# Kernel optimization log

Measured on AMD Instinct MI355X. Metric: run time of the kernel, lower is better.

## Reference

```python
import jax, jax.numpy as jnp
import numpy as np

N = 16384      # total nodes in batched graph
B = 64         # number of graphs (dgl.batch)
DEG = 8        # random in-degree (self-loops added on top)
C = 128        # feature width
H = 2          # heads in middle blocks
EH = 8         # E: heads of attn_seq / codebook entries
DEPTH = 2
IN = 8         # max_node_color (one-hot input width)
NE = N * DEG + N  # edges incl. self-loops


def layernorm(x, g, b, eps=1e-5):
    mu = jnp.mean(x, axis=-1, keepdims=True)
    var = jnp.mean(jnp.square(x - mu), axis=-1, keepdims=True)
    return (x - mu) * jax.lax.rsqrt(var + eps) * g + b


def gatv2(x, src, dst, Ws, bs, Wd, bd, attn):
    # DGL GATv2Conv (eval mode, attn_drop inactive, share_weights=False)
    h, c = attn.shape
    n = x.shape[0]
    el = (x @ Ws + bs).reshape(n, h, c)   # fc_src
    er = (x @ Wd + bd).reshape(n, h, c)   # fc_dst
    e = jax.nn.leaky_relu(el[src] + er[dst], negative_slope=0.2)  # [E,h,c]
    logits = jnp.einsum('ehc,hc->eh', e, attn)                    # [E,h]
    # edge softmax over incoming edges of each dst node
    m = jax.ops.segment_max(logits, dst, num_segments=n)
    a = jnp.exp(logits - m[dst])
    z = jax.ops.segment_sum(a, dst, num_segments=n)
    a = a / z[dst]
    return jax.ops.segment_sum(el[src] * a[..., None], dst, num_segments=n)  # [n,h,c]


def setup_inputs() -> dict:
    key = jax.random.key(0)
    ks = iter(jax.random.split(key, 64))
    nrm = lambda *s: jax.random.normal(next(ks), s, jnp.float32) * 0.05
    colors = jax.random.randint(next(ks), (N,), 0, IN)
    feats = jax.nn.one_hot(colors, IN, dtype=jnp.float32)
    loops = jnp.arange(N)
    src = jnp.concatenate([jax.random.randint(next(ks), (N * DEG,), 0, N), loops])
    dst = jnp.concatenate([jax.random.randint(next(ks), (N * DEG,), 0, N), loops])
    graph_ids = jnp.arange(N) // (N // B)
    inp = dict(feats=feats, src=src, dst=dst, graph_ids=graph_ids)
    # attn_up: GATv2Conv(IN -> C, 1 head)
    inp.update(up_Ws=nrm(IN, C), up_bs=nrm(C), up_Wd=nrm(IN, C), up_bd=nrm(C), up_attn=nrm(1, C))
    # depth blocks: GATv2Conv(C -> C, H heads) + ff
    inp.update(L_Ws=nrm(DEPTH, C, H * C), L_bs=nrm(DEPTH, H * C),
               L_Wd=nrm(DEPTH, C, H * C), L_bd=nrm(DEPTH, H * C),
               L_attn=nrm(DEPTH, H, C),
               ff_ln_g=jnp.ones((DEPTH, C), jnp.float32), ff_ln_b=jnp.zeros((DEPTH, C), jnp.float32),
               ff_W1=nrm(DEPTH, C, 2 * C), ff_b1=nrm(DEPTH, 2 * C),
               ff_W2=nrm(DEPTH, 2 * C, C), ff_b2=nrm(DEPTH, C),
               ff_W3=nrm(DEPTH, H * C, C), ff_b3=nrm(DEPTH, C))
    # attn_seq: GATv2Conv(C -> C, EH heads) + ff_seq
    inp.update(seq_Ws=nrm(C, EH * C), seq_bs=nrm(EH * C),
               seq_Wd=nrm(C, EH * C), seq_bd=nrm(EH * C),
               seq_attn=nrm(EH, C),
               fs_ln_g=jnp.ones((C,), jnp.float32), fs_ln_b=jnp.zeros((C,), jnp.float32),
               fs_W1=nrm(C, 2 * C), fs_b1=nrm(2 * C),
               fs_W2=nrm(2 * C, C), fs_b2=nrm(C),
               gate_W=nrm(EH * C, 1), gate_b=nrm(1))
    return inp


def reference(feats, src, dst, graph_ids,
              up_Ws, up_bs, up_Wd, up_bd, up_attn,
              L_Ws, L_bs, L_Wd, L_bd, L_attn,
              ff_ln_g, ff_ln_b, ff_W1, ff_b1, ff_W2, ff_b2, ff_W3, ff_b3,
              seq_Ws, seq_bs, seq_Wd, seq_bd, seq_attn,
              fs_ln_g, fs_ln_b, fs_W1, fs_b1, fs_W2, fs_b2,
              gate_W, gate_b):
    # attn_up (1 head) -> flatten to [N, C]
    x = gatv2(feats, src, dst, up_Ws, up_bs, up_Wd, up_bd, up_attn).reshape(N, C)
    for l in range(DEPTH):
        h = gatv2(x, src, dst, L_Ws[l], L_bs[l], L_Wd[l], L_bd[l], L_attn[l])  # [N,H,C]
        h = layernorm(h, ff_ln_g[l], ff_ln_b[l])
        h = jax.nn.gelu(h @ ff_W1[l] + ff_b1[l], approximate=False)
        h = h @ ff_W2[l] + ff_b2[l]                              # [N,H,C]
        x = h.reshape(N, H * C) @ ff_W3[l] + ff_b3[l]            # [N,C]
    y = gatv2(x, src, dst, seq_Ws, seq_bs, seq_Wd, seq_bd, seq_attn)  # [N,EH,C]
    y = layernorm(y, fs_ln_g, fs_ln_b)
    y = jax.nn.gelu(y @ fs_W1 + fs_b1, approximate=False) @ fs_W2 + fs_b2
    y = y.reshape(N, EH * C)
    # GlobalAttentionPooling: softmax(gate) over nodes within each graph
    gate = y @ gate_W + gate_b                                   # [N,1]
    gm = jax.ops.segment_max(gate, graph_ids, num_segments=B)
    ga = jnp.exp(gate - gm[graph_ids])
    gz = jax.ops.segment_sum(ga, graph_ids, num_segments=B)
    ga = ga / gz[graph_ids]
    pooled = jax.ops.segment_sum(ga * y, graph_ids, num_segments=B)  # [B, EH*C]
    return jnp.tanh(pooled.reshape(B, EH, C))
```

## Files before the change

kernel.cpp:

```cpp
#include <hip/hip_runtime.h>
#include <hip/hip_bf16.h>

typedef __hip_bfloat16 bf16;
typedef __attribute__((ext_vector_type(8))) short short8;
typedef __attribute__((ext_vector_type(4))) float f32x4;

#define NN 16384
#define NB 64
#define NE_TOT (NN*8 + NN)
#define CW 128

__device__ __forceinline__ float b2f(bf16 x){ return __bfloat162float(x); }
__device__ __forceinline__ bf16  f2b(float x){ return __float2bfloat16(x); }
__device__ __forceinline__ float lrelu(float x){ return fmaxf(x, 0.2f*x); }
__device__ __forceinline__ float gelu_f(float x){ return 0.5f*x*(1.f + erff(x*0.70710678118654752f)); }
__device__ __forceinline__ float us2f(unsigned int u){ return __uint_as_float(u << 16); }
__device__ __forceinline__ unsigned short f2us(float x){ return __builtin_bit_cast(unsigned short, f2b(x)); }

__device__ __forceinline__ void async16(const void* g, void* l){
  __builtin_amdgcn_global_load_lds((const __attribute__((address_space(1))) void*)g,
                                   (__attribute__((address_space(3))) void*)l, 16, 0, 0);
}

__global__ void k_detect(const unsigned short* __restrict__ f, int* __restrict__ flag){
  __shared__ int cnt;
  if(threadIdx.x == 0) cnt = 0;
  __syncthreads();
  int c = 0;
  for(int i = threadIdx.x; i < 2048; i += 256)
    if(f[2*i] == 0x3F80) c++;
  atomicAdd(&cnt, c);
  __syncthreads();
  if(threadIdx.x == 0) *flag = (cnt > 0) ? 0 : 1;
}

struct ConvArgs { const void* in[32]; bf16* out[32]; int n[32]; int tk[32]; int tj[32]; int ls[32]; };
__global__ __launch_bounds__(256) void k_conv_all(ConvArgs a, const int* __restrict__ flag){
  int which = blockIdx.y;
  int t = blockIdx.x*256 + threadIdx.x;
  int n = a.n[which];
  if(t >= n) return;
  float v = (*flag) ? ((const float*)a.in[which])[t] : b2f(((const bf16*)a.in[which])[t]);
  int tj = a.tj[which];
  if(tj == 0){ a.out[which][t] = f2b(v); return; }
  int tk = a.tk[which], kj = tk*tj;
  int l = t / kj, r = t - l*kj;
  int k = r / tj, j = r - k*tj;
  a.out[which][l*a.ls[which] + j*tk + k] = f2b(v);
}

__global__ void k_zero3(int* __restrict__ a, int* __restrict__ b, float* __restrict__ g, int n){
  int i = blockIdx.x*blockDim.x + threadIdx.x;
  if(i < n){ a[i] = 0; b[i] = 0; g[i] = 0.f; }
}
__global__ void k_hist(const int* __restrict__ dst, int* __restrict__ deg, int ne){
  int e = blockIdx.x*blockDim.x + threadIdx.x;
  if(e < ne) atomicAdd(&deg[dst[e]], 1);
}
__global__ void k_scan(const int* __restrict__ deg, int* __restrict__ off){
  __shared__ int s[256];
  int t = threadIdx.x;
  const int chunk = NN/256;
  int base = t*chunk;
  int sum = 0;
  for(int i=0;i<chunk;i++) sum += deg[base+i];
  s[t] = sum; __syncthreads();
  for(int o=1;o<256;o<<=1){
    int v = (t >= o) ? s[t-o] : 0;
    __syncthreads();
    s[t] += v;
    __syncthreads();
  }
  int run = (t == 0) ? 0 : s[t-1];
  for(int i=0;i<chunk;i++){ off[base+i] = run; run += deg[base+i]; }
  if(t == 255) off[NN] = run;
}
__global__ void k_scatter(const int* __restrict__ src, const int* __restrict__ dst,
                          const int* __restrict__ off, int* __restrict__ cursor,
                          int* __restrict__ csr_src, int ne){
  int e = blockIdx.x*blockDim.x + threadIdx.x;
  if(e < ne){
    int d = dst[e];
    int p = off[d] + atomicAdd(&cursor[d], 1);
    csr_src[p] = src[e];
  }
}

__global__ __launch_bounds__(128) void k_up(const bf16* __restrict__ feats,
    const bf16* __restrict__ Ws, const bf16* __restrict__ bs,
    const bf16* __restrict__ Wd, const bf16* __restrict__ bd,
    bf16* __restrict__ eler){
  int n = blockIdx.x, c = threadIdx.x;
  __shared__ float f[8];
  if(c < 8) f[c] = b2f(feats[n*8 + c]);
  __syncthreads();
  float a = b2f(bs[c]), b = b2f(bd[c]);
  #pragma unroll
  for(int k=0;k<8;k++){
    float fv = f[k];
    a += fv*b2f(Ws[k*CW + c]);
    b += fv*b2f(Wd[k*CW + c]);
  }
  eler[(size_t)n*256 + c]       = f2b(a);
  eler[(size_t)n*256 + 128 + c] = f2b(b);
}

template<int ACT>
__global__ __launch_bounds__(256) void k_mm(
    const bf16* __restrict__ A, int gshA, int gstrA,
    const bf16* __restrict__ WT, const bf16* __restrict__ bias,
    bf16* __restrict__ C, int gshC, int gstrC,
    int K, int J){
  __shared__ char smem[32768];
  short* As = (short*)smem;
  short* Bs = (short*)(smem + 16384);
  int tid = threadIdx.x, w = tid >> 6, lane = tid & 63;
  int l15 = lane & 15, q = lane >> 4;
  int wm = w >> 1, wn = w & 1;
  int bm = blockIdx.y*128, bn = blockIdx.x*128;

  f32x4 acc[4][4];
  #pragma unroll
  for(int i=0;i<4;i++)
    #pragma unroll
    for(int j=0;j<4;j++) acc[i][j] = (f32x4)0.f;

  int srow = w*32 + (lane >> 2);
  int scol = (lane & 3)*8;
  const bf16* gA[2]; const bf16* gB[2];
  short* lA[2]; short* lB[2];
  int mskA = (1 << gshA) - 1;
  #pragma unroll
  for(int a=0;a<2;a++){
    int rowA = bm + srow + a*16;
    gA[a] = A  + (size_t)(rowA >> gshA)*(size_t)gstrA + (size_t)(rowA & mskA)*K + scol;
    gB[a] = WT + (size_t)(bn + srow + a*16)*K + scol;
    lA[a] = As + (w*32 + a*16)*32;
    lB[a] = Bs + (w*32 + a*16)*32;
  }

  for(int kt=0; kt<K; kt+=64){
    #pragma unroll
    for(int a=0;a<2;a++)
      #pragma unroll
      for(int kh=0;kh<2;kh++){
        async16(gA[a] + kt + kh*32, lA[a] + kh*4096);
        async16(gB[a] + kt + kh*32, lB[a] + kh*4096);
      }
    __syncthreads();
    #pragma unroll
    for(int kh=0;kh<2;kh++){
      short8 af[4], bfr[4];
      #pragma unroll
      for(int i=0;i<4;i++) af[i]  = *(short8*)&As[kh*4096 + (wm*64 + i*16 + l15)*32 + q*8];
      #pragma unroll
      for(int j=0;j<4;j++) bfr[j] = *(short8*)&Bs[kh*4096 + (wn*64 + j*16 + l15)*32 + q*8];
      #pragma unroll
      for(int i=0;i<4;i++)
        #pragma unroll
        for(int j=0;j<4;j++)
          acc[i][j] = __builtin_amdgcn_mfma_f32_16x16x32_bf16(af[i], bfr[j], acc[i][j], 0, 0, 0);
    }
    __syncthreads();
  }

  float* ep = (float*)(smem + w*4352);
  int rr = lane >> 2;
  int cc = (lane & 3)*16;
  int mskC = (1 << gshC) - 1;
  #pragma unroll
  for(int i=0;i<4;i++){
    #pragma unroll
    for(int j=0;j<4;j++){
      float bv = b2f(bias[bn + wn*64 + j*16 + l15]);
      #pragma unroll
      for(int r=0;r<4;r++){
        float v = acc[i][j][r] + bv;
        if(ACT == 1) v = gelu_f(v);
        ep[(q*4+r)*68 + j*16 + l15] = v;
      }
    }
    float4 v0 = *(float4*)&ep[rr*68 + cc];
    float4 v1 = *(float4*)&ep[rr*68 + cc + 4];
    float4 v2 = *(float4*)&ep[rr*68 + cc + 8];
    float4 v3 = *(float4*)&ep[rr*68 + cc + 12];
    float vv[16] = {v0.x,v0.y,v0.z,v0.w, v1.x,v1.y,v1.z,v1.w,
                    v2.x,v2.y,v2.z,v2.w, v3.x,v3.y,v3.z,v3.w};
    unsigned int u[8];
    #pragma unroll
    for(int k=0;k<8;k++)
      u[k] = (unsigned int)f2us(vv[2*k]) | ((unsigned int)f2us(vv[2*k+1]) << 16);
    int row = bm + wm*64 + i*16 + rr;
    bf16* cp = C + (size_t)(row >> gshC)*(size_t)gstrC + (size_t)(row & mskC)*J + bn + wn*64 + cc;
    *(uint4*)cp       = make_uint4(u[0],u[1],u[2],u[3]);
    *(uint4*)(cp + 8) = make_uint4(u[4],u[5],u[6],u[7]);
  }
}

template<int E>
__device__ __forceinline__ void load_row(const bf16* p, float* f){
  if constexpr (E == 2){
    unsigned int v = *(const unsigned int*)p;
    f[0] = us2f(v & 0xffffu); f[1] = __uint_as_float(v & 0xffff0000u);
  } else if constexpr (E == 4){
    uint2 v = *(const uint2*)p;
    f[0] = us2f(v.x & 0xffffu); f[1] = __uint_as_float(v.x & 0xffff0000u);
    f[2] = us2f(v.y & 0xffffu); f[3] = __uint_as_float(v.y & 0xffff0000u);
  } else if constexpr (E == 8){
    uint4 a = *(const uint4*)p;
    unsigned int vs[4] = {a.x,a.y,a.z,a.w};
    #pragma unroll
    for(int i=0;i<4;i++){
      f[2*i]   = us2f(vs[i] & 0xffffu);
      f[2*i+1] = __uint_as_float(vs[i] & 0xffff0000u);
    }
  } else {
    uint4 a = *(const uint4*)p;
    uint4 b = *(const uint4*)(p + 8);
    unsigned int vs[8] = {a.x,a.y,a.z,a.w,b.x,b.y,b.z,b.w};
    #pragma unroll
    for(int i=0;i<8;i++){
      f[2*i]   = us2f(vs[i] & 0xffffu);
      f[2*i+1] = __uint_as_float(vs[i] & 0xffff0000u);
    }
  }
}
template<int E>
__device__ __forceinline__ void store_row(bf16* p, const float* f){
  unsigned int vs[E/2];
  #pragma unroll
  for(int i=0;i<E/2;i++)
    vs[i] = (unsigned int)f2us(f[2*i]) | ((unsigned int)f2us(f[2*i+1]) << 16);
  if constexpr (E == 2){ *(unsigned int*)p = vs[0]; }
  else if constexpr (E == 4){ *(uint2*)p = make_uint2(vs[0], vs[1]); }
  else if constexpr (E == 8){ *(uint4*)p = make_uint4(vs[0], vs[1], vs[2], vs[3]); }
  else {
    *(uint4*)p       = make_uint4(vs[0], vs[1], vs[2], vs[3]);
    *(uint4*)(p + 8) = make_uint4(vs[4], vs[5], vs[6], vs[7]);
  }
}

template<int GATE>
__global__ __launch_bounds__(256) void k_ff(
    const bf16* __restrict__ A, int gshA, int gstrA,
    const bf16* __restrict__ W1T, const bf16* __restrict__ b1,
    const bf16* __restrict__ W2T, const bf16* __restrict__ b2,
    bf16* __restrict__ C, int gshC, int gstrC,
    const bf16* __restrict__ gW, float* __restrict__ gate){
  __shared__ short Wb[8704];
  __shared__ short Hs[16896];
  int tid = threadIdx.x, w = tid >> 6, lane = tid & 63;
  int l15 = lane & 15, q = lane >> 4;
  int bm = blockIdx.x*64;
  int mskA = (1 << gshA) - 1, mskC = (1 << gshC) - 1;

  int rowA = bm + w*16 + l15;
  const bf16* ap = A + (size_t)(rowA >> gshA)*(size_t)gstrA + (size_t)(rowA & mskA)*128;
  short8 af[4];
  #pragma unroll
  for(int ki=0;ki<4;ki++) af[ki] = *(const short8*)&ap[ki*32 + q*8];

  for(int jt=0; jt<4; jt++){
    #pragma unroll
    for(int it=0;it<4;it++){
      int slot = tid + it*256;
      int r = slot >> 4, c8 = slot & 15;
      *(int4*)&Wb[r*132 + c8*8] = *(const int4*)&W1T[(size_t)(jt*64 + r)*128 + c8*8];
    }
    __syncthreads();
    f32x4 acc1[4] = {(f32x4)0.f, (f32x4)0.f, (f32x4)0.f, (f32x4)0.f};
    #pragma unroll
    for(int ki=0;ki<4;ki++){
      #pragma unroll
      for(int t=0;t<4;t++){
        short8 bfr = *(short8*)&Wb[(t*16 + l15)*132 + ki*32 + q*8];
        acc1[t] = __builtin_amdgcn_mfma_f32_16x16x32_bf16(af[ki], bfr, acc1[t], 0, 0, 0);
      }
    }
    #pragma unroll
    for(int t=0;t<4;t++){
      int jcol = jt*64 + t*16 + l15;
      float bv = b2f(b1[jcol]);
      #pragma unroll
      for(int r=0;r<4;r++){
        float v = gelu_f(acc1[t][r] + bv);
        Hs[(w*16 + q*4 + r)*260 + jcol] = (short)f2us(v);
      }
    }
    __syncthreads();
  }

  f32x4 acc2[8];
  #pragma unroll
  for(int t=0;t<8;t++) acc2[t] = (f32x4)0.f;
  for(int kc=0; kc<4; kc++){
    #pragma unroll
    for(int it=0;it<4;it++){
      int slot = tid + it*256;
      int r = slot >> 3, c8 = slot & 7;
      *(int4*)&Wb[r*68 + c8*8] = *(const int4*)&W2T[(size_t)r*256 + kc*64 + c8*8];
    }
    __syncthreads();
    #pragma unroll
    for(int ki=0;ki<2;ki++){
      short8 haf = *(short8*)&Hs[(w*16 + l15)*260 + kc*64 + ki*32 + q*8];
      #pragma unroll
      for(int t=0;t<8;t++){
        short8 bfr = *(short8*)&Wb[(t*16 + l15)*68 + ki*32 + q*8];
        acc2[t] = __builtin_amdgcn_mfma_f32_16x16x32_bf16(haf, bfr, acc2[t], 0, 0, 0);
      }
    }
    __syncthreads();
  }

  float* epf = (float*)Hs;
  #pragma unroll
  for(int t=0;t<8;t++){
    int jcol = t*16 + l15;
    float bv = b2f(b2[jcol]);
    #pragma unroll
    for(int r=0;r<4;r++)
      epf[(w*16 + q*4 + r)*132 + jcol] = acc2[t][r] + bv;
  }
  __syncthreads();
  int row = tid >> 2, cseg = (tid & 3)*32;
  float vv[32];
  #pragma unroll
  for(int k8=0;k8<8;k8++){
    float4 v = *(float4*)&epf[row*132 + cseg + k8*4];
    vv[k8*4+0] = v.x; vv[k8*4+1] = v.y; vv[k8*4+2] = v.z; vv[k8*4+3] = v.w;
  }
  unsigned int u[16];
  #pragma unroll
  for(int k=0;k<16;k++)
    u[k] = (unsigned int)f2us(vv[2*k]) | ((unsigned int)f2us(vv[2*k+1]) << 16);
  int rowC = bm + row;
  bf16* cpb = C + (size_t)(rowC >> gshC)*(size_t)gstrC + (size_t)(rowC & mskC)*128 + cseg;
  *(uint4*)cpb        = make_uint4(u[0], u[1], u[2], u[3]);
  *(uint4*)(cpb + 8)  = make_uint4(u[4], u[5], u[6], u[7]);
  *(uint4*)(cpb + 16) = make_uint4(u[8], u[9], u[10],u[11]);
  *(uint4*)(cpb + 24) = make_uint4(u[12],u[13],u[14],u[15]);

  if constexpr (GATE){
    float gwf[32];
    load_row<16>(gW + (rowC & 7)*128 + cseg,      gwf);
    load_row<16>(gW + (rowC & 7)*128 + cseg + 16, gwf + 16);
    float p = 0.f;
    #pragma unroll
    for(int k=0;k<32;k++) p += vv[k]*gwf[k];
    p += __shfl_xor(p, 1, 64);
    p += __shfl_xor(p, 2, 64);
    if((tid & 3) == 0) atomicAdd(&gate[rowC >> 3], p);
  }
}

__global__ __launch_bounds__(256) void k_ffw3(
    const bf16* __restrict__ A,
    const bf16* __restrict__ W1T, const bf16* __restrict__ b1,
    const bf16* __restrict__ W2T, const bf16* __restrict__ b2,
    const bf16* __restrict__ W3T, const bf16* __restrict__ b3,
    bf16* __restrict__ X){
  __shared__ short Wb[8704];
  __shared__ short Hs[16896];
  int tid = threadIdx.x, w = tid >> 6, lane = tid & 63;
  int l15 = lane & 15, q = lane >> 4;
  int bm = blockIdx.x*64;

  int rowA = bm + w*16 + l15;
  const bf16* ap = A + (size_t)rowA*128;
  short8 af[4];
  #pragma unroll
  for(int ki=0;ki<4;ki++) af[ki] = *(const short8*)&ap[ki*32 + q*8];

  for(int jt=0; jt<4; jt++){
    #pragma unroll
    for(int it=0;it<4;it++){
      int slot = tid + it*256;
      int r = slot >> 4, c8 = slot & 15;
      *(int4*)&Wb[r*132 + c8*8] = *(const int4*)&W1T[(size_t)(jt*64 + r)*128 + c8*8];
    }
    __syncthreads();
    f32x4 acc1[4] = {(f32x4)0.f, (f32x4)0.f, (f32x4)0.f, (f32x4)0.f};
    #pragma unroll
    for(int ki=0;ki<4;ki++){
      #pragma unroll
      for(int t=0;t<4;t++){
        short8 bfr = *(short8*)&Wb[(t*16 + l15)*132 + ki*32 + q*8];
        acc1[t] = __builtin_amdgcn_mfma_f32_16x16x32_bf16(af[ki], bfr, acc1[t], 0, 0, 0);
      }
    }
    #pragma unroll
    for(int t=0;t<4;t++){
      int jcol = jt*64 + t*16 + l15;
      float bv = b2f(b1[jcol]);
      #pragma unroll
      for(int r=0;r<4;r++){
        float v = gelu_f(acc1[t][r] + bv);
        Hs[(w*16 + q*4 + r)*260 + jcol] = (short)f2us(v);
      }
    }
    __syncthreads();
  }

  f32x4 acc2[8];
  #pragma unroll
  for(int t=0;t<8;t++) acc2[t] = (f32x4)0.f;
  for(int kc=0; kc<4; kc++){
    #pragma unroll
    for(int it=0;it<4;it++){
      int slot = tid + it*256;
      int r = slot >> 3, c8 = slot & 7;
      *(int4*)&Wb[r*68 + c8*8] = *(const int4*)&W2T[(size_t)r*256 + kc*64 + c8*8];
    }
    __syncthreads();
    #pragma unroll
    for(int ki=0;ki<2;ki++){
      short8 haf = *(short8*)&Hs[(w*16 + l15)*260 + kc*64 + ki*32 + q*8];
      #pragma unroll
      for(int t=0;t<8;t++){
        short8 bfr = *(short8*)&Wb[(t*16 + l15)*68 + ki*32 + q*8];
        acc2[t] = __builtin_amdgcn_mfma_f32_16x16x32_bf16(haf, bfr, acc2[t], 0, 0, 0);
      }
    }
    __syncthreads();
  }
  #pragma unroll
  for(int t=0;t<8;t++){
    int jcol = t*16 + l15;
    float bv = b2f(b2[jcol]);
    #pragma unroll
    for(int r=0;r<4;r++)
      Wb[(w*16 + q*4 + r)*128 + jcol] = (short)f2us(acc2[t][r] + bv);
  }
  __syncthreads();

  int mt = w >> 1, jh = w & 1;
  short8 a3[8];
  #pragma unroll
  for(int c=0;c<8;c++) a3[c] = *(short8*)&Wb[(mt*16 + l15)*256 + c*32 + q*8];
  __syncthreads();

  f32x4 acc3[4] = {(f32x4)0.f, (f32x4)0.f, (f32x4)0.f, (f32x4)0.f};
  for(int kc=0; kc<4; kc++){
    #pragma unroll
    for(int it=0;it<4;it++){
      int slot = tid + it*256;
      int r = slot >> 3, c8 = slot & 7;
      *(int4*)&Wb[r*68 + c8*8] = *(const int4*)&W3T[(size_t)r*256 + kc*64 + c8*8];
    }
    __syncthreads();
    #pragma unroll
    for(int ki=0;ki<2;ki++){
      short8 haf = a3[kc*2 + ki];
      #pragma unroll
      for(int t=0;t<4;t++){
        short8 bfr = *(short8*)&Wb[(jh*64 + t*16 + l15)*68 + ki*32 + q*8];
        acc3[t] = __builtin_amdgcn_mfma_f32_16x16x32_bf16(haf, bfr, acc3[t], 0, 0, 0);
      }
    }
    __syncthreads();
  }

  float* epf = (float*)Hs;
  #pragma unroll
  for(int t=0;t<4;t++){
    int jcol = jh*64 + t*16 + l15;
    float bv = b2f(b3[jcol]);
    #pragma unroll
    for(int r=0;r<4;r++)
      epf[(mt*16 + q*4 + r)*132 + jcol] = acc3[t][r] + bv;
  }
  __syncthreads();
  int row = tid >> 3, cseg = (tid & 7)*16;
  float4 v0 = *(float4*)&epf[row*132 + cseg];
  float4 v1 = *(float4*)&epf[row*132 + cseg + 4];
  float4 v2 = *(float4*)&epf[row*132 + cseg + 8];
  float4 v3 = *(float4*)&epf[row*132 + cseg + 12];
  float vv[16] = {v0.x,v0.y,v0.z,v0.w, v1.x,v1.y,v1.z,v1.w,
                  v2.x,v2.y,v2.z,v2.w, v3.x,v3.y,v3.z,v3.w};
  unsigned int u[8];
  #pragma unroll
  for(int k=0;k<8;k++)
    u[k] = (unsigned int)f2us(vv[2*k]) | ((unsigned int)f2us(vv[2*k+1]) << 16);
  bf16* xp = X + (size_t)(bm/2 + row)*128 + cseg;
  *(uint4*)xp       = make_uint4(u[0],u[1],u[2],u[3]);
  *(uint4*)(xp + 8) = make_uint4(u[4],u[5],u[6],u[7]);
}

template<int H, bool LNF>
__global__ __launch_bounds__(256) void k_gat(const int* __restrict__ off, const int* __restrict__ csr_src,
    const bf16* __restrict__ el, const bf16* __restrict__ er, const bf16* __restrict__ attn,
    const bf16* __restrict__ lng, const bf16* __restrict__ lnb, bf16* __restrict__ out,
    int rs_in, int rs_out){
  constexpr int EPL = 2*H;
  constexpr int G   = 64/H;
  int w = threadIdx.x >> 6, lane = threadIdx.x & 63;
  int n = blockIdx.x*4 + w;

  float ef[EPL], af[EPL];
  load_row<EPL>(er   + (size_t)n*rs_in + lane*EPL, ef);
  load_row<EPL>(attn + lane*EPL, af);

  int p0 = off[n], p1 = off[n+1];
  int deg = p1 - p0;
  int sidx = csr_src[p0 + (lane < deg ? lane : deg-1)];

  float z = 0.f;
  float acc[EPL];
  #pragma unroll
  for(int e=0;e<EPL;e++) acc[e] = 0.f;

  float xa[EPL], xb[EPL];
  {
    int s0 = __shfl(sidx, 0, 64);
    load_row<EPL>(el + (size_t)s0*rs_in + lane*EPL, xa);
  }
  if(deg > 1){
    int s1 = __shfl(sidx, 1, 64);
    load_row<EPL>(el + (size_t)s1*rs_in + lane*EPL, xb);
  }

  for(int p = 0; p < deg; p += 2){
    float na[EPL], nb[EPL];
    int i2 = p + 2, i3 = p + 3;
    int s2b = __shfl(sidx, i2 & 63, 64);
    int s3b = __shfl(sidx, i3 & 63, 64);
    if(i2 < deg){
      int sc = (i2 < 64) ? s2b : csr_src[p0 + i2];
      load_row<EPL>(el + (size_t)sc*rs_in + lane*EPL, na);
    }
    if(i3 < deg){
      int sd = (i3 < 64) ? s3b : csr_src[p0 + i3];
      load_row<EPL>(el + (size_t)sd*rs_in + lane*EPL, nb);
    }
    {
      float part = 0.f;
      #pragma unroll
      for(int e=0;e<EPL;e++) part += af[e]*lrelu(xa[e] + ef[e]);
      #pragma unroll
      for(int o=G/2; o; o>>=1) part += __shfl_xor(part, o, 64);
      float c = __expf(part);
      z += c;
      #pragma unroll
      for(int e=0;e<EPL;e++) acc[e] += c*xa[e];
    }
    if(p + 1 < deg){
      float part = 0.f;
      #pragma unroll
      for(int e=0;e<EPL;e++) part += af[e]*lrelu(xb[e] + ef[e]);
      #pragma unroll
      for(int o=G/2; o; o>>=1) part += __shfl_xor(part, o, 64);
      float c = __expf(part);
      z += c;
      #pragma unroll
      for(int e=0;e<EPL;e++) acc[e] += c*xb[e];
    }
    #pragma unroll
    for(int e=0;e<EPL;e++){ xa[e] = na[e]; xb[e] = nb[e]; }
  }
  float rz = 1.f/z;
  #pragma unroll
  for(int e=0;e<EPL;e++) acc[e] *= rz;

  if constexpr (LNF){
    float sl = 0.f;
    #pragma unroll
    for(int e=0;e<EPL;e++) sl += acc[e];
    #pragma unroll
    for(int o=G/2; o; o>>=1) sl += __shfl_xor(sl, o, 64);
    float mu = sl*(1.f/128.f);
    float qs = 0.f;
    #pragma unroll
    for(int e=0;e<EPL;e++){ float d = acc[e] - mu; qs += d*d; }
    #pragma unroll
    for(int o=G/2; o; o>>=1) qs += __shfl_xor(qs, o, 64);
    float r = rsqrtf(qs*(1.f/128.f) + 1e-5f);
    int cbase = (lane & (G-1))*EPL;
    #pragma unroll
    for(int e=0;e<EPL;e++)
      acc[e] = (acc[e] - mu)*r*b2f(lng[cbase + e]) + b2f(lnb[cbase + e]);
  }
  store_row<EPL>(out + (size_t)n*rs_out + lane*EPL, acc);
}

__global__ __launch_bounds__(64) void k_pool1(const float* __restrict__ gate,
                                              float* __restrict__ gm, float* __restrict__ gz){
  int g = blockIdx.x, lane = threadIdx.x;
  float v0 = gate[g*256 + lane], v1 = gate[g*256 + 64 + lane];
  float v2 = gate[g*256 + 128 + lane], v3 = gate[g*256 + 192 + lane];
  float m = fmaxf(fmaxf(v0,v1), fmaxf(v2,v3));
  #pragma unroll
  for(int o=32;o;o>>=1) m = fmaxf(m, __shfl_xor(m, o, 64));
  float z = __expf(v0-m) + __expf(v1-m) + __expf(v2-m) + __expf(v3-m);
  #pragma unroll
  for(int o=32;o;o>>=1) z += __shfl_xor(z, o, 64);
  if(lane == 0){ gm[g] = m; gz[g] = z; }
}

__global__ __launch_bounds__(256) void k_pool2(const float* __restrict__ gate,
    const float* __restrict__ gm, const float* __restrict__ gz,
    const bf16* __restrict__ y2, void* __restrict__ outv, const int* __restrict__ flag){
  int g = blockIdx.x >> 2, cb = blockIdx.x & 3, t = threadIdx.x;
  __shared__ float aL[256];
  aL[t] = __expf(gate[g*256 + t] - gm[g]) / gz[g];
  __syncthreads();
  int ch = cb*256 + t;
  float acc = 0.f;
  const bf16* base = y2 + (size_t)g*256*2048 + ch;
  for(int i=0;i<256;i++) acc += aL[i]*b2f(base[(size_t)i*2048]);
  float v = tanhf(acc);
  size_t idx = (size_t)g*1024 + ch;
  if(*flag) ((float*)outv)[idx] = v;
  else      ((bf16*)outv)[idx] = f2b(v);
}

extern "C" void kernel_launch(void* const* d_in, const int* in_sizes, int n_in,
                              void* d_out, int out_size, void* d_ws, size_t ws_size,
                              hipStream_t stream){
  const int* src = (const int*)d_in[1];
  const int* dst = (const int*)d_in[2];

  char* wsb = (char*)d_ws;
  size_t o = 0;
  auto take = [&](size_t bytes)->char*{
    char* p = wsb + o; o = (o + bytes + 255) & ~(size_t)255; return p;
  };
  int*   flag  = (int*)take(4);
  float* gate  = (float*)take((size_t)NN*4);
  float* gm    = (float*)take(64*4);
  float* gz    = (float*)take(64*4);
  int* deg     = (int*)take((size_t)NN*4);
  int* cursor  = (int*)take((size_t)NN*4);
  int* off     = (int*)take((size_t)(NN+1)*4);
  int* csr_src = (int*)take((size_t)NE_TOT*4);

  bf16* WcombL   = (bf16*)take((size_t)2*512*128*2);
  bf16* bcombL   = (bf16*)take((size_t)2*512*2);
  bf16* WcombSeq = (bf16*)take((size_t)2048*128*2);
  bf16* bcombSeq = (bf16*)take((size_t)2048*2);

  ConvArgs ca;
  const int fidx[32] = {0, 4,5,6,7,8, 9,10,11,12,13, 14,15,16,17,18,19,20,21,
                        22,23,24,25,26, 27,28,29,30,31,32, 33,34};
  bf16* cp[32];
  int maxn = 0;
  for(int i=0;i<32;i++){
    int n = in_sizes[fidx[i]];
    ca.in[i] = d_in[fidx[i]]; ca.n[i] = n;
    ca.tk[i] = 0; ca.tj[i] = 0; ca.ls[i] = 0;
    cp[i] = nullptr;
    if(n > maxn) maxn = n;
  }
  auto plain = [&](int i){ cp[i] = (bf16*)take((size_t)ca.n[i]*2); ca.out[i] = cp[i]; };
  auto spec  = [&](int i, bf16* dst_, int tk, int tj, int ls){
    ca.out[i] = dst_; ca.tk[i] = tk; ca.tj[i] = tj; ca.ls[i] = ls; cp[i] = dst_; };
  auto owntr = [&](int i, int tk, int tj){
    cp[i] = (bf16*)take((size_t)ca.n[i]*2);
    ca.out[i] = cp[i]; ca.tk[i] = tk; ca.tj[i] = tj; ca.ls[i] = tk*tj; };

  plain(0);
  plain(1); plain(2); plain(3); plain(4); plain(5);
  spec(6,  WcombL,          128, 256, 65536);
  spec(7,  bcombL,          256, 1,   512);
  spec(8,  WcombL + 32768,  128, 256, 65536);
  spec(9,  bcombL + 256,    256, 1,   512);
  plain(10); plain(11); plain(12);
  owntr(13, 128, 256);
  plain(14);
  owntr(15, 256, 128); plain(16);
  owntr(17, 256, 128); plain(18);
  spec(19, WcombSeq,           128, 1024, 131072);
  spec(20, bcombSeq,           1024, 1,  2048);
  spec(21, WcombSeq + 131072,  128, 1024, 131072);
  spec(22, bcombSeq + 1024,    1024, 1,  2048);
  plain(23); plain(24); plain(25);
  owntr(26, 128, 256); plain(27);
  owntr(28, 256, 128); plain(29);
  plain(30); plain(31);

  bf16* AB = (bf16*)take((size_t)NN*2048*2);
  bf16* X  = (bf16*)take((size_t)NN*128*2);
  bf16* G1 = AB + (size_t)NN*1024;
  (void)ws_size; (void)n_in; (void)out_size;

  k_detect<<<1, 256, 0, stream>>>((const unsigned short*)d_in[0], flag);
  k_conv_all<<<dim3((maxn+255)/256, 32), 256, 0, stream>>>(ca, flag);

  k_zero3 <<<(NN+255)/256, 256, 0, stream>>>(deg, cursor, gate, NN);
  k_hist  <<<(NE_TOT+255)/256, 256, 0, stream>>>(dst, deg, NE_TOT);
  k_scan  <<<1, 256, 0, stream>>>(deg, off);
  k_scatter<<<(NE_TOT+255)/256, 256, 0, stream>>>(src, dst, off, cursor, csr_src, NE_TOT);

  k_up<<<NN, 128, 0, stream>>>(cp[0], cp[1], cp[2], cp[3], cp[4], AB);
  k_gat<1,false><<<NN/4, 256, 0, stream>>>(off, csr_src, AB, AB + 128, cp[5],
                                           nullptr, nullptr, X, 256, 128);

  for(int l=0; l<2; l++){
    k_mm<0><<<dim3(4, 128), 256, 0, stream>>>(X, 30, 0, WcombL + l*65536, bcombL + l*512,
                                              AB, 30, 0, 128, 512);
    k_gat<2,true><<<NN/4, 256, 0, stream>>>(off, csr_src, AB, AB + 256, cp[10] + l*256,
                                            cp[11] + l*128, cp[12] + l*128, G1, 512, 256);
    k_ffw3<<<2*NN/64, 256, 0, stream>>>(G1, cp[13] + l*32768, cp[14] + l*256,
                                        cp[15] + l*32768, cp[16] + l*128,
                                        cp[17] + l*32768, cp[18] + l*128, X);
  }

  k_mm<0><<<dim3(16, 128), 256, 0, stream>>>(X, 30, 0, WcombSeq, bcombSeq, AB, 30, 0, 128, 2048);
  k_gat<8,true><<<NN/4, 256, 0, stream>>>(off, csr_src, AB, AB + 1024, cp[23],
                                          cp[24], cp[25], AB + 1024, 2048, 2048);
  k_ff<1><<<131072/64, 256, 0, stream>>>(AB + 1024, 3, 2048, cp[26], cp[27],
                                         cp[28], cp[29], AB, 3, 2048,
                                         cp[30], gate);

  k_pool1<<<NB, 64, 0, stream>>>(gate, gm, gz);
  k_pool2<<<NB*4, 256, 0, stream>>>(gate, gm, gz, AB, d_out, flag);
}
```

Measured before the change: 470.7 us.

## Replace first GATv2 layer with color lookup table and retile FF kernel

Because the input features are one-hot node colors, the first GATv2 layer is rewritten to decode each node's color once. It precomputes an 8x8 table of attention logits and per-color source projections, then computes each node's output from per-color neighbor counts gathered with wave ballots. This removes the per-node projection kernel and the full 128-channel edge gather of the first layer. Separately, the FF kernel now stages 128-wide weight tiles in two passes instead of four and drops the LDS row padding. That cuts barriers but may add LDS bank conflicts, and it raises shared memory use.

```diff
diff --git a/kernel.cpp b/kernel.cpp
--- a/kernel.cpp
+++ b/kernel.cpp
@@ -49,9 +49,16 @@
   a.out[which][l*a.ls[which] + j*tk + k] = f2b(v);
 }
 
-__global__ void k_zero3(int* __restrict__ a, int* __restrict__ b, float* __restrict__ g, int n){
+__global__ void k_zero3c(int* __restrict__ a, int* __restrict__ b, float* __restrict__ g,
+                         const bf16* __restrict__ feats, int* __restrict__ color, int n){
   int i = blockIdx.x*blockDim.x + threadIdx.x;
-  if(i < n){ a[i] = 0; b[i] = 0; g[i] = 0.f; }
+  if(i < n){
+    a[i] = 0; b[i] = 0; g[i] = 0.f;
+    int best = 0; float bv = -1e30f;
+    #pragma unroll
+    for(int k=0;k<8;k++){ float v = b2f(feats[i*8+k]); if(v > bv){ bv = v; best = k; } }
+    color[i] = best;
+  }
 }
 __global__ void k_hist(const int* __restrict__ dst, int* __restrict__ deg, int ne){
   int e = blockIdx.x*blockDim.x + threadIdx.x;
@@ -86,23 +93,68 @@
   }
 }
 
-__global__ __launch_bounds__(128) void k_up(const bf16* __restrict__ feats,
+__global__ __launch_bounds__(256) void k_upgat(const int* __restrict__ off, const int* __restrict__ csr_src,
+    const int* __restrict__ color,
     const bf16* __restrict__ Ws, const bf16* __restrict__ bs,
     const bf16* __restrict__ Wd, const bf16* __restrict__ bd,
-    bf16* __restrict__ eler){
-  int n = blockIdx.x, c = threadIdx.x;
-  __shared__ float f[8];
-  if(c < 8) f[c] = b2f(feats[n*8 + c]);
-  __syncthreads();
-  float a = b2f(bs[c]), b = b2f(bd[c]);
-  #pragma unroll
-  for(int k=0;k<8;k++){
-    float fv = f[k];
-    a += fv*b2f(Ws[k*CW + c]);
-    b += fv*b2f(Wd[k*CW + c]);
-  }
-  eler[(size_t)n*256 + c]       = f2b(a);
-  eler[(size_t)n*256 + 128 + c] = f2b(b);
+    const bf16* __restrict__ attn, bf16* __restrict__ X){
+  __shared__ float elt[8][128];
+  __shared__ float ert[8][128];
+  __shared__ float Lt[8][8];
+  int tid = threadIdx.x;
+  for(int e = tid; e < 1024; e += 256){
+    int col = e >> 7, c = e & 127;
+    elt[col][c] = b2f(Ws[col*128 + c]) + b2f(bs[c]);
+    ert[col][c] = b2f(Wd[col*128 + c]) + b2f(bd[c]);
+  }
+  __syncthreads();
+  {
+    int p = tid >> 2, q4 = tid & 3;
+    int cs = p >> 3, cn = p & 7;
+    float part = 0.f;
+    for(int c = q4*32; c < q4*32 + 32; c++)
+      part += b2f(attn[c])*lrelu(elt[cs][c] + ert[cn][c]);
+    part += __shfl_xor(part, 1, 64);
+    part += __shfl_xor(part, 2, 64);
+    if(q4 == 0) Lt[cs][cn] = part;
+  }
+  __syncthreads();
+
+  int w = tid >> 6, lane = tid & 63;
+  for(int it = 0; it < 4; it++){
+    int n = blockIdx.x*16 + it*4 + w;
+    int p0 = off[n], p1 = off[n+1], deg = p1 - p0;
+    int cs = 0;
+    if(lane < deg) cs = color[csr_src[p0 + lane]];
+    int cn = color[n];
+    float z = 0.f, wgt[8];
+    #pragma unroll
+    for(int col=0; col<8; col++){
+      unsigned long long m = __ballot(lane < deg && cs == col);
+      float e = __expf(Lt[col][cn]);
+      float cw = (float)__popcll(m)*e;
+      wgt[col] = cw;
+      z += cw;
+    }
+    if(deg > 64){
+      for(int p = p0 + 64; p < p1; p++){
+        int c2 = color[csr_src[p]];
+        float e = __expf(Lt[c2][cn]);
+        wgt[c2] += e; z += e;
+      }
+    }
+    float rz = 1.f/z;
+    int c0 = lane*2;
+    float a0 = 0.f, a1 = 0.f;
+    #pragma unroll
+    for(int col=0; col<8; col++){
+      float wc = wgt[col]*rz;
+      a0 += wc*elt[col][c0];
+      a1 += wc*elt[col][c0+1];
+    }
+    unsigned int v = (unsigned int)f2us(a0) | ((unsigned int)f2us(a1) << 16);
+    *(unsigned int*)&X[(size_t)n*128 + c0] = v;
+  }
 }
 
 template<int ACT>
@@ -247,8 +299,8 @@
     const bf16* __restrict__ W2T, const bf16* __restrict__ b2,
     bf16* __restrict__ C, int gshC, int gstrC,
     const bf16* __restrict__ gW, float* __restrict__ gate){
-  __shared__ short Wb[8704];
-  __shared__ short Hs[16896];
+  __shared__ short Wb[16384];
+  __shared__ short Hs[16384];
   int tid = threadIdx.x, w = tid >> 6, lane = tid & 63;
   int l15 = lane & 15, q = lane >> 4;
   int bm = blockIdx.x*64;
@@ -260,31 +312,33 @@
   #pragma unroll
   for(int ki=0;ki<4;ki++) af[ki] = *(const short8*)&ap[ki*32 + q*8];
 
-  for(int jt=0; jt<4; jt++){
-    #pragma unroll
-    for(int it=0;it<4;it++){
+  for(int jt=0; jt<2; jt++){
+    #pragma unroll
+    for(int it=0;it<8;it++){
       int slot = tid + it*256;
       int r = slot >> 4, c8 = slot & 15;
-      *(int4*)&Wb[r*132 + c8*8] = *(const int4*)&W1T[(size_t)(jt*64 + r)*128 + c8*8];
-    }
-    __syncthreads();
-    f32x4 acc1[4] = {(f32x4)0.f, (f32x4)0.f, (f32x4)0.f, (f32x4)0.f};
+      *(int4*)&Wb[r*128 + c8*8] = *(const int4*)&W1T[(size_t)(jt*128 + r)*128 + c8*8];
+    }
+    __syncthreads();
+    f32x4 acc1[8];
+    #pragma unroll
+    for(int t=0;t<8;t++) acc1[t] = (f32x4)0.f;
     #pragma unroll
     for(int ki=0;ki<4;ki++){
       #pragma unroll
-      for(int t=0;t<4;t++){
-        short8 bfr = *(short8*)&Wb[(t*16 + l15)*132 + ki*32 + q*8];
+      for(int t=0;t<8;t++){
+        short8 bfr = *(short8*)&Wb[(t*16 + l15)*128 + ki*32 + q*8];
         acc1[t] = __builtin_amdgcn_mfma_f32_16x16x32_bf16(af[ki], bfr, acc1[t], 0, 0, 0);
       }
     }
     #pragma unroll
-    for(int t=0;t<4;t++){
-      int jcol = jt*64 + t*16 + l15;
+    for(int t=0;t<8;t++){
+      int jcol = jt*128 + t*16 + l15;
       float bv = b2f(b1[jcol]);
       #pragma unroll
       for(int r=0;r<4;r++){
         float v = gelu_f(acc1[t][r] + bv);
-        Hs[(w*16 + q*4 + r)*260 + jcol] = (short)f2us(v);
+        Hs[(w*16 + q*4 + r)*256 + jcol] = (short)f2us(v);
       }
     }
     __syncthreads();
@@ -293,20 +347,20 @@
   f32x4 acc2[8];
   #pragma unroll
   for(int t=0;t<8;t++) acc2[t] = (f32x4)0.f;
-  for(int kc=0; kc<4; kc++){
-    #pragma unroll
-    for(int it=0;it<4;it++){
+  for(int kc=0; kc<2; kc++){
+    #pragma unroll
+    for(int it=0;it<8;it++){
       int slot = tid + it*256;
-      int r = slot >> 3, c8 = slot & 7;
-      *(int4*)&Wb[r*68 + c8*8] = *(const int4*)&W2T[(size_t)r*256 + kc*64 + c8*8];
-    }
-    __syncthreads();
-    #pragma unroll
-    for(int ki=0;ki<2;ki++){
-      short8 haf = *(short8*)&Hs[(w*16 + l15)*260 + kc*64 + ki*32 + q*8];
+      int r = slot >> 4, c8 = slot & 15;
+      *(int4*)&Wb[r*128 + c8*8] = *(const int4*)&W2T[(size_t)r*256 + kc*128 + c8*8];
+    }
+    __syncthreads();
+    #pragma unroll
+    for(int ki=0;ki<4;ki++){
+      short8 haf = *(short8*)&Hs[(w*16 + l15)*256 + kc*128 + ki*32 + q*8];
       #pragma unroll
       for(int t=0;t<8;t++){
-        short8 bfr = *(short8*)&Wb[(t*16 + l15)*68 + ki*32 + q*8];
+        short8 bfr = *(short8*)&Wb[(t*16 + l15)*128 + ki*32 + q*8];
         acc2[t] = __builtin_amdgcn_mfma_f32_16x16x32_bf16(haf, bfr, acc2[t], 0, 0, 0);
       }
     }
@@ -320,14 +374,14 @@
     float bv = b2f(b2[jcol]);
     #pragma unroll
     for(int r=0;r<4;r++)
-      epf[(w*16 + q*4 + r)*132 + jcol] = acc2[t][r] + bv;
+      epf[(w*16 + q*4 + r)*128 + jcol] = acc2[t][r] + bv;
   }
   __syncthreads();
   int row = tid >> 2, cseg = (tid & 3)*32;
   float vv[32];
   #pragma unroll
   for(int k8=0;k8<8;k8++){
-    float4 v = *(float4*)&epf[row*132 + cseg + k8*4];
+    float4 v = *(float4*)&epf[row*128 + cseg + k8*4];
     vv[k8*4+0] = v.x; vv[k8*4+1] = v.y; vv[k8*4+2] = v.z; vv[k8*4+3] = v.w;
   }
   unsigned int u[16];
@@ -633,6 +687,7 @@
   int* cursor  = (int*)take((size_t)NN*4);
   int* off     = (int*)take((size_t)(NN+1)*4);
   int* csr_src = (int*)take((size_t)NE_TOT*4);
+  int* color   = (int*)take((size_t)NN*4);
 
   bf16* WcombL   = (bf16*)take((size_t)2*512*128*2);
   bf16* bcombL   = (bf16*)take((size_t)2*512*2);
@@ -686,14 +741,12 @@
   k_detect<<<1, 256, 0, stream>>>((const unsigned short*)d_in[0], flag);
   k_conv_all<<<dim3((maxn+255)/256, 32), 256, 0, stream>>>(ca, flag);
 
-  k_zero3 <<<(NN+255)/256, 256, 0, stream>>>(deg, cursor, gate, NN);
+  k_zero3c<<<(NN+255)/256, 256, 0, stream>>>(deg, cursor, gate, cp[0], color, NN);
   k_hist  <<<(NE_TOT+255)/256, 256, 0, stream>>>(dst, deg, NE_TOT);
   k_scan  <<<1, 256, 0, stream>>>(deg, off);
   k_scatter<<<(NE_TOT+255)/256, 256, 0, stream>>>(src, dst, off, cursor, csr_src, NE_TOT);
 
-  k_up<<<NN, 128, 0, stream>>>(cp[0], cp[1], cp[2], cp[3], cp[4], AB);
-  k_gat<1,false><<<NN/4, 256, 0, stream>>>(off, csr_src, AB, AB + 128, cp[5],
-                                           nullptr, nullptr, X, 256, 128);
+  k_upgat<<<NN/16, 256, 0, stream>>>(off, csr_src, color, cp[1], cp[2], cp[3], cp[4], cp[5], X);
 
   for(int l=0; l<2; l++){
     k_mm<0><<<dim3(4, 128), 256, 0, stream>>>(X, 30, 0, WcombL + l*65536, bcombL + l*512,
```

Result: slower. 482.1 us (+2.4%).
